# Performance work log

Measured on AMD Instinct MI355X. Metric: run time of the kernel, lower is better.

Reference implementation:

```python
import jax, jax.numpy as jnp
import numpy as np

EMB = 64
HID = 128
N_NODES = 50000
N_EDGES = 800000
N_Q = 64

def setup_inputs() -> dict:
    key = jax.random.key(0)
    ks = jax.random.split(key, 20)
    d = {}
    d['question_emb'] = jax.random.normal(ks[0], (N_Q, EMB), dtype=jnp.float32)
    d['node_embeddings'] = jax.random.normal(ks[1], (N_NODES, EMB), dtype=jnp.float32)
    d['edge_embeddings'] = jax.random.normal(ks[2], (N_EDGES, EMB), dtype=jnp.float32)
    d['edge_index'] = jax.random.randint(ks[3], (2, N_EDGES), 0, N_NODES, dtype=jnp.int32)
    d['node_batch'] = jnp.sort(jax.random.randint(ks[4], (N_NODES,), 0, N_Q, dtype=jnp.int32))
    s = 1.0 / np.sqrt(EMB)
    # projector weights (Linear emb->emb), stored as (in, out)
    d['Wq'] = jax.random.normal(ks[5], (EMB, EMB), dtype=jnp.float32) * s
    d['bq'] = jnp.zeros((EMB,), dtype=jnp.float32)
    d['We'] = jax.random.normal(ks[6], (EMB, EMB), dtype=jnp.float32) * s
    d['be'] = jnp.zeros((EMB,), dtype=jnp.float32)
    d['Wr'] = jax.random.normal(ks[7], (EMB, EMB), dtype=jnp.float32) * s
    d['br'] = jnp.zeros((EMB,), dtype=jnp.float32)
    # DenseFeatureExtractor: concat(4*EMB) -> EMB -> HID, ReLU after each
    d['W1'] = jax.random.normal(ks[8], (4 * EMB, EMB), dtype=jnp.float32) / np.sqrt(4 * EMB)
    d['b1'] = jnp.zeros((EMB,), dtype=jnp.float32)
    d['W2'] = jax.random.normal(ks[9], (EMB, HID), dtype=jnp.float32) * s
    d['b2'] = jnp.zeros((HID,), dtype=jnp.float32)
    # DeterministicHead: HID -> 1
    d['Wh'] = jax.random.normal(ks[10], (HID, 1), dtype=jnp.float32) / np.sqrt(HID)
    d['bh'] = jnp.zeros((1,), dtype=jnp.float32)
    return d


def reference(question_emb, node_embeddings, edge_embeddings, edge_index, node_batch,
              Wq, bq, We, be, Wr, br, W1, b1, W2, b2, Wh, bh):
    head_idx, tail_idx = edge_index[0], edge_index[1]
    query_ids = node_batch[head_idx]                       # [E]
    # projections (applied to the small tables, then gathered per edge)
    q_repr = question_emb @ Wq + bq                        # [Q, D]
    node_repr = node_embeddings @ We + be                  # [N, D]
    rel_repr = edge_embeddings @ Wr + br                   # [E, D]
    semantic = jnp.concatenate([
        q_repr[query_ids], node_repr[head_idx], rel_repr, node_repr[tail_idx]
    ], axis=-1)                                            # [E, 4D]
    h = jax.nn.relu(semantic @ W1 + b1)                    # [E, D]
    h = jax.nn.relu(h @ W2 + b2)                           # [E, H]
    logits = (h @ Wh + bh)[:, 0]                           # [E]
    scores = jax.nn.sigmoid(logits)
    return scores
```

## Files before the change

kernel.cpp:

```cpp
#include <hip/hip_runtime.h>

#define NNODE 50000
#define NEDGE 800000

typedef __attribute__((ext_vector_type(8))) short bf16x8;
typedef __attribute__((ext_vector_type(4))) float f32x4;

#define WB_QCB   0
#define WB_WRTB  8192
#define WB_W2TB  16384
#define WB_WEH   33024
#define WB_WET   49408
#define WB_NHB   65792
#define WB_NTB   6465792

__device__ inline ushort f2b(float x) {
    uint u = __float_as_uint(x);
    return (ushort)((u + 0x7fffu + ((u >> 16) & 1u)) >> 16);
}
__device__ inline float bLo(uint u) { return __uint_as_float(u << 16); }
__device__ inline float bHi(uint u) { return __uint_as_float(u & 0xffff0000u); }

__device__ inline void stage64(float* dst, const float* __restrict__ src, int t) {
    #pragma unroll
    for (int i = 0; i < 4; ++i) {
        int f = t + i * 256;
        *(float4*)&dst[f * 4] = *(const float4*)&src[f * 4];
    }
}

__device__ inline void gemm64(const float* sA, const float* sB, int t, float acc[4][4]) {
    const int r0 = (t >> 4) * 4, c0 = (t & 15) * 4;
    #pragma unroll
    for (int j = 0; j < 4; ++j)
        #pragma unroll
        for (int i = 0; i < 4; ++i) acc[j][i] = 0.f;
    #pragma unroll 4
    for (int k = 0; k < 64; ++k) {
        float4 b = *(const float4*)&sB[k * 64 + c0];
        float bv[4] = {b.x, b.y, b.z, b.w};
        #pragma unroll
        for (int j = 0; j < 4; ++j) {
            float a = sA[(r0 + j) * 64 + k];
            #pragma unroll
            for (int i = 0; i < 4; ++i) acc[j][i] = fmaf(a, bv[i], acc[j][i]);
        }
    }
}

__global__ __launch_bounds__(256)
void prep_small(const float* __restrict__ Q,
                const float* __restrict__ Wq, const float* __restrict__ bq,
                const float* __restrict__ We, const float* __restrict__ be,
                const float* __restrict__ Wr, const float* __restrict__ br,
                const float* __restrict__ W1, const float* __restrict__ b1,
                const float* __restrict__ W2, char* __restrict__ wsb)
{
    __shared__ float sA[4096], sB[4096], sC[4096], sBias[64];
    const int t = threadIdx.x;
    const int bid = blockIdx.x;
    const int r0 = (t >> 4) * 4, c0 = (t & 15) * 4;

    if (bid == 0) {
        stage64(sA, Wq, t); stage64(sB, W1, t);
        __syncthreads();
        float acc[4][4];
        gemm64(sA, sB, t, acc);
        #pragma unroll
        for (int j = 0; j < 4; ++j)
            *(float4*)&sC[(r0 + j) * 64 + c0] = make_float4(acc[j][0], acc[j][1], acc[j][2], acc[j][3]);
        if (t < 64) {
            float s = b1[t];
            for (int k = 0; k < 64; ++k) {
                s = fmaf(bq[k], W1[k * 64 + t], s);
                s = fmaf(be[k], W1[(64 + k) * 64 + t] + W1[(192 + k) * 64 + t], s);
                s = fmaf(br[k], W1[(128 + k) * 64 + t], s);
            }
            sBias[t] = s;
        }
        __syncthreads();
        stage64(sA, Q, t);
        __syncthreads();
        gemm64(sA, sC, t, acc);
        ushort* qcb = (ushort*)(wsb + WB_QCB);
        #pragma unroll
        for (int j = 0; j < 4; ++j) {
            ushort4 p;
            p.x = f2b(acc[j][0] + sBias[c0 + 0]);
            p.y = f2b(acc[j][1] + sBias[c0 + 1]);
            p.z = f2b(acc[j][2] + sBias[c0 + 2]);
            p.w = f2b(acc[j][3] + sBias[c0 + 3]);
            *(ushort4*)&qcb[(r0 + j) * 64 + c0] = p;
        }
    } else if (bid == 1 || bid == 2) {
        const float* w1seg = W1 + (bid == 1 ? 64 * 64 : 192 * 64);
        float* dst = (float*)(wsb + (bid == 1 ? WB_WEH : WB_WET));
        stage64(sA, We, t); stage64(sB, w1seg, t);
        __syncthreads();
        float acc[4][4];
        gemm64(sA, sB, t, acc);
        #pragma unroll
        for (int j = 0; j < 4; ++j)
            *(float4*)&dst[(r0 + j) * 64 + c0] = make_float4(acc[j][0], acc[j][1], acc[j][2], acc[j][3]);
    } else if (bid == 3) {
        stage64(sA, Wr, t); stage64(sB, W1 + 128 * 64, t);
        __syncthreads();
        float acc[4][4];
        gemm64(sA, sB, t, acc);
        ushort* wrtb = (ushort*)(wsb + WB_WRTB);
        #pragma unroll
        for (int j = 0; j < 4; ++j)
            #pragma unroll
            for (int i = 0; i < 4; ++i)
                wrtb[(c0 + i) * 64 + (r0 + j)] = f2b(acc[j][i]);
    } else {
        ushort* w2tb = (ushort*)(wsb + WB_W2TB);
        #pragma unroll
        for (int i = 0; i < 32; ++i) {
            int f = t + i * 256;
            int k = f >> 7, n = f & 127;
            w2tb[n * 64 + k] = f2b(W2[f]);
        }
    }
}

__global__ __launch_bounds__(256)
void prep_nodes(const float* __restrict__ Xn, const char* __restrict__ wsb_c,
                char* __restrict__ wsb)
{
    __shared__ float sXT[64 * 68];
    __shared__ float sWeh[4096], sWet[4096];
    const int t = threadIdx.x;
    const int nbase = blockIdx.x * 64;
    const float* Weh = (const float*)(wsb_c + WB_WEH);
    const float* Wet = (const float*)(wsb_c + WB_WET);
    ushort* nhb = (ushort*)(wsb + WB_NHB);
    ushort* ntb = (ushort*)(wsb + WB_NTB);

    #pragma unroll
    for (int i = 0; i < 4; ++i) {
        int f = t + i * 256;
        int n = f >> 4, s4 = (f & 15) * 4;
        int gn = nbase + n;
        float4 v = make_float4(0.f, 0.f, 0.f, 0.f);
        if (gn < NNODE) v = *(const float4*)&Xn[gn * 64 + s4];
        sXT[(s4 + 0) * 68 + n] = v.x;
        sXT[(s4 + 1) * 68 + n] = v.y;
        sXT[(s4 + 2) * 68 + n] = v.z;
        sXT[(s4 + 3) * 68 + n] = v.w;
    }
    #pragma unroll
    for (int i = 0; i < 4; ++i) {
        int f = t + i * 256;
        *(float4*)&sWeh[f * 4] = *(const float4*)&Weh[f * 4];
        *(float4*)&sWet[f * 4] = *(const float4*)&Wet[f * 4];
    }
    __syncthreads();

    const int er = (t >> 4) * 4, cc = (t & 15) * 4;
    float ah[4][4], at[4][4];
    #pragma unroll
    for (int j = 0; j < 4; ++j)
        #pragma unroll
        for (int i = 0; i < 4; ++i) { ah[j][i] = 0.f; at[j][i] = 0.f; }
    #pragma unroll 4
    for (int k = 0; k < 64; ++k) {
        float4 a  = *(const float4*)&sXT[k * 68 + er];
        float4 bh = *(const float4*)&sWeh[k * 64 + cc];
        float4 bt = *(const float4*)&sWet[k * 64 + cc];
        float av[4] = {a.x, a.y, a.z, a.w};
        #pragma unroll
        for (int j = 0; j < 4; ++j) {
            ah[j][0] = fmaf(av[j], bh.x, ah[j][0]); ah[j][1] = fmaf(av[j], bh.y, ah[j][1]);
            ah[j][2] = fmaf(av[j], bh.z, ah[j][2]); ah[j][3] = fmaf(av[j], bh.w, ah[j][3]);
            at[j][0] = fmaf(av[j], bt.x, at[j][0]); at[j][1] = fmaf(av[j], bt.y, at[j][1]);
            at[j][2] = fmaf(av[j], bt.z, at[j][2]); at[j][3] = fmaf(av[j], bt.w, at[j][3]);
        }
    }
    #pragma unroll
    for (int j = 0; j < 4; ++j) {
        int n = nbase + er + j;
        if (n < NNODE) {
            ushort4 ph, pt;
            ph.x = f2b(ah[j][0]); ph.y = f2b(ah[j][1]); ph.z = f2b(ah[j][2]); ph.w = f2b(ah[j][3]);
            pt.x = f2b(at[j][0]); pt.y = f2b(at[j][1]); pt.z = f2b(at[j][2]); pt.w = f2b(at[j][3]);
            *(ushort4*)&nhb[n * 64 + cc] = ph;
            *(ushort4*)&ntb[n * 64 + cc] = pt;
        }
    }
}

__global__ __launch_bounds__(256, 3)
void edge_kernel(const float* __restrict__ Xe,
                 const int* __restrict__ EI,
                 const int* __restrict__ NB,
                 const float* __restrict__ b2,
                 const float* __restrict__ Wh,
                 const float* __restrict__ bh,
                 const char* __restrict__ wsb,
                 float* __restrict__ out)
{
    __shared__ ushort sX[64 * 72];
    __shared__ ushort sWr[64 * 72];
    __shared__ ushort sW2[128 * 72];
    __shared__ ushort sG[64 * 72];
    __shared__ float  sB2s[128], sWhs[128];

    const int t = threadIdx.x;
    const int ebase = blockIdx.x * 64;
    const ushort* qcb  = (const ushort*)(wsb + WB_QCB);
    const ushort* wrtb = (const ushort*)(wsb + WB_WRTB);
    const ushort* w2tb = (const ushort*)(wsb + WB_W2TB);
    const ushort* nhb  = (const ushort*)(wsb + WB_NHB);
    const ushort* ntb  = (const ushort*)(wsb + WB_NTB);

    const int eg = t >> 2;
    const int c0 = (t & 3) * 16;
    int hd = EI[ebase + eg];
    int tl = EI[NEDGE + ebase + eg];
    int qi = NB[hd];
    uint4 ga0 = *(const uint4*)&qcb[qi * 64 + c0];
    uint4 ga1 = *(const uint4*)&qcb[qi * 64 + c0 + 8];
    uint4 gb0 = *(const uint4*)&nhb[hd * 64 + c0];
    uint4 gb1 = *(const uint4*)&nhb[hd * 64 + c0 + 8];
    uint4 gc0 = *(const uint4*)&ntb[tl * 64 + c0];
    uint4 gc1 = *(const uint4*)&ntb[tl * 64 + c0 + 8];

    float4 xv[4];
    #pragma unroll
    for (int i = 0; i < 4; ++i) {
        int f = t + i * 256;
        xv[i] = *(const float4*)&Xe[(ebase + (f >> 4)) * 64 + (f & 15) * 4];
    }
    uint4 wrl[2], w2l[4];
    #pragma unroll
    for (int i = 0; i < 2; ++i) {
        int f = t + i * 256;
        wrl[i] = *(const uint4*)&wrtb[(f >> 3) * 64 + (f & 7) * 8];
    }
    #pragma unroll
    for (int i = 0; i < 4; ++i) {
        int f = t + i * 256;
        w2l[i] = *(const uint4*)&w2tb[(f >> 3) * 64 + (f & 7) * 8];
    }
    if (t < 128) { sB2s[t] = b2[t]; sWhs[t] = Wh[t]; }
    float bh0 = bh[0];

    {
        uint pk[8];
        const uint* ua = (const uint*)&ga0; const uint* ub = (const uint*)&gb0;
        const uint* uc = (const uint*)&gc0;
        #pragma unroll
        for (int j = 0; j < 4; ++j) {
            float lo = bLo(ua[j]) + bLo(ub[j]) + bLo(uc[j]);
            float hi = bHi(ua[j]) + bHi(ub[j]) + bHi(uc[j]);
            pk[j] = (uint)f2b(lo) | ((uint)f2b(hi) << 16);
        }
        ua = (const uint*)&ga1; ub = (const uint*)&gb1; uc = (const uint*)&gc1;
        #pragma unroll
        for (int j = 0; j < 4; ++j) {
            float lo = bLo(ua[j]) + bLo(ub[j]) + bLo(uc[j]);
            float hi = bHi(ua[j]) + bHi(ub[j]) + bHi(uc[j]);
            pk[4 + j] = (uint)f2b(lo) | ((uint)f2b(hi) << 16);
        }
        *(uint4*)&sG[eg * 72 + c0]     = make_uint4(pk[0], pk[1], pk[2], pk[3]);
        *(uint4*)&sG[eg * 72 + c0 + 8] = make_uint4(pk[4], pk[5], pk[6], pk[7]);
    }
    #pragma unroll
    for (int i = 0; i < 4; ++i) {
        int f = t + i * 256;
        int e = f >> 4, s4 = (f & 15) * 4;
        uint lo = (uint)f2b(xv[i].x) | ((uint)f2b(xv[i].y) << 16);
        uint hi = (uint)f2b(xv[i].z) | ((uint)f2b(xv[i].w) << 16);
        *(uint2*)&sX[e * 72 + s4] = make_uint2(lo, hi);
    }
    #pragma unroll
    for (int i = 0; i < 2; ++i) {
        int f = t + i * 256;
        *(uint4*)&sWr[(f >> 3) * 72 + (f & 7) * 8] = wrl[i];
    }
    #pragma unroll
    for (int i = 0; i < 4; ++i) {
        int f = t + i * 256;
        *(uint4*)&sW2[(f >> 3) * 72 + (f & 7) * 8] = w2l[i];
    }
    __syncthreads();

    const int lane = t & 63;
    const int w = t >> 6;
    const int m = lane & 15;
    const int qq = lane >> 4;
    const int q8 = qq * 8;

    bf16x8 a0 = *(const bf16x8*)&sX[(w * 16 + m) * 72 + q8];
    bf16x8 a1 = *(const bf16x8*)&sX[(w * 16 + m) * 72 + 32 + q8];
    f32x4 acc1[4];
    #pragma unroll
    for (int nt = 0; nt < 4; ++nt) {
        bf16x8 b0 = *(const bf16x8*)&sWr[(nt * 16 + m) * 72 + q8];
        bf16x8 b1v = *(const bf16x8*)&sWr[(nt * 16 + m) * 72 + 32 + q8];
        f32x4 c = {0.f, 0.f, 0.f, 0.f};
        c = __builtin_amdgcn_mfma_f32_16x16x32_bf16(a0, b0, c, 0, 0, 0);
        c = __builtin_amdgcn_mfma_f32_16x16x32_bf16(a1, b1v, c, 0, 0, 0);
        acc1[nt] = c;
    }
    ushort h1s[4][4];
    #pragma unroll
    for (int nt = 0; nt < 4; ++nt) {
        int c = nt * 16 + m;
        #pragma unroll
        for (int r = 0; r < 4; ++r) {
            int e = w * 16 + qq * 4 + r;
            float gv = __uint_as_float(((uint)sG[e * 72 + c]) << 16);
            h1s[nt][r] = f2b(fmaxf(acc1[nt][r] + gv, 0.f));
        }
    }
    __syncthreads();
    #pragma unroll
    for (int nt = 0; nt < 4; ++nt) {
        int c = nt * 16 + m;
        #pragma unroll
        for (int r = 0; r < 4; ++r) {
            int e = w * 16 + qq * 4 + r;
            sX[e * 72 + c] = h1s[nt][r];
        }
    }
    __syncthreads();

    bf16x8 A0 = *(const bf16x8*)&sX[(w * 16 + m) * 72 + q8];
    bf16x8 A1 = *(const bf16x8*)&sX[(w * 16 + m) * 72 + 32 + q8];
    float part[4] = {0.f, 0.f, 0.f, 0.f};
    #pragma unroll
    for (int nt = 0; nt < 8; ++nt) {
        bf16x8 B0 = *(const bf16x8*)&sW2[(nt * 16 + m) * 72 + q8];
        bf16x8 B1 = *(const bf16x8*)&sW2[(nt * 16 + m) * 72 + 32 + q8];
        f32x4 c = {0.f, 0.f, 0.f, 0.f};
        c = __builtin_amdgcn_mfma_f32_16x16x32_bf16(A0, B0, c, 0, 0, 0);
        c = __builtin_amdgcn_mfma_f32_16x16x32_bf16(A1, B1, c, 0, 0, 0);
        int col = nt * 16 + m;
        float b2v = sB2s[col], whv = sWhs[col];
        #pragma unroll
        for (int r = 0; r < 4; ++r)
            part[r] = fmaf(fmaxf(c[r] + b2v, 0.f), whv, part[r]);
    }
    #pragma unroll
    for (int md = 1; md < 16; md <<= 1) {
        part[0] += __shfl_xor(part[0], md, 64);
        part[1] += __shfl_xor(part[1], md, 64);
        part[2] += __shfl_xor(part[2], md, 64);
        part[3] += __shfl_xor(part[3], md, 64);
    }
    if (m == 0) {
        float4 o;
        o.x = 1.f / (1.f + __expf(-(part[0] + bh0)));
        o.y = 1.f / (1.f + __expf(-(part[1] + bh0)));
        o.z = 1.f / (1.f + __expf(-(part[2] + bh0)));
        o.w = 1.f / (1.f + __expf(-(part[3] + bh0)));
        *(float4*)&out[ebase + w * 16 + qq * 4] = o;
    }
}

extern "C" void kernel_launch(void* const* d_in, const int* in_sizes, int n_in,
                              void* d_out, int out_size, void* d_ws, size_t ws_size,
                              hipStream_t stream)
{
    const float* Q   = (const float*)d_in[0];
    const float* Xn  = (const float*)d_in[1];
    const float* Xe  = (const float*)d_in[2];
    const int*   EI  = (const int*)d_in[3];
    const int*   NB  = (const int*)d_in[4];
    const float* Wq  = (const float*)d_in[5];
    const float* bq  = (const float*)d_in[6];
    const float* We  = (const float*)d_in[7];
    const float* be  = (const float*)d_in[8];
    const float* Wr  = (const float*)d_in[9];
    const float* br  = (const float*)d_in[10];
    const float* W1  = (const float*)d_in[11];
    const float* b1  = (const float*)d_in[12];
    const float* W2  = (const float*)d_in[13];
    const float* b2  = (const float*)d_in[14];
    const float* Wh  = (const float*)d_in[15];
    const float* bh  = (const float*)d_in[16];
    float* out = (float*)d_out;
    char*  wsb = (char*)d_ws;

    prep_small<<<5, 256, 0, stream>>>(Q, Wq, bq, We, be, Wr, br, W1, b1, W2, wsb);
    prep_nodes<<<(NNODE + 63) / 64, 256, 0, stream>>>(Xn, wsb, wsb);
    edge_kernel<<<NEDGE / 64, 256, 0, stream>>>(Xe, EI, NB, b2, Wh, bh, wsb, out);
}
```

Before: 375.1 us.

## Load MFMA operands directly into registers and permute hidden layout to cut LDS syncs

The edge kernel now loads the edge-embedding A fragments and Wr B fragments straight from global memory into registers in MFMA layout, so the sX and sWr shared buffers are gone. The gathered sum is stored in a permuted column order, and W2 rows are permuted to match. This lets each wave write its first-layer output to a wave-private sH region with packed stores and read it back with no extra block barriers. Less LDS is used, so occupancy is raised to 4 blocks per SIMD, at the cost of uncoalesced per-lane global loads and more register pressure.

```diff
diff --git a/kernel.cpp b/kernel.cpp
--- a/kernel.cpp
+++ b/kernel.cpp
@@ -18,8 +18,13 @@
     uint u = __float_as_uint(x);
     return (ushort)((u + 0x7fffu + ((u >> 16) & 1u)) >> 16);
 }
+__device__ inline uint pack2(float lo, float hi) {
+    return (uint)f2b(lo) | ((uint)f2b(hi) << 16);
+}
 __device__ inline float bLo(uint u) { return __uint_as_float(u << 16); }
 __device__ inline float bHi(uint u) { return __uint_as_float(u & 0xffff0000u); }
+
+union B8U { uint4 u; bf16x8 b; };
 
 __device__ inline void stage64(float* dst, const float* __restrict__ src, int t) {
     #pragma unroll
@@ -119,7 +124,7 @@
         for (int i = 0; i < 32; ++i) {
             int f = t + i * 256;
             int k = f >> 7, n = f & 127;
-            w2tb[n * 64 + k] = f2b(W2[f]);
+            w2tb[n * 64 + ((k & 15) * 4 + (k >> 4))] = f2b(W2[f]);
         }
     }
 }
@@ -190,7 +195,7 @@
     }
 }
 
-__global__ __launch_bounds__(256, 3)
+__global__ __launch_bounds__(256, 4)
 void edge_kernel(const float* __restrict__ Xe,
                  const int* __restrict__ EI,
                  const int* __restrict__ NB,
@@ -200,135 +205,100 @@
                  const char* __restrict__ wsb,
                  float* __restrict__ out)
 {
-    __shared__ ushort sX[64 * 72];
-    __shared__ ushort sWr[64 * 72];
+    __shared__ ushort sG[64 * 72];
+    __shared__ ushort sH[64 * 72];
     __shared__ ushort sW2[128 * 72];
-    __shared__ ushort sG[64 * 72];
     __shared__ float  sB2s[128], sWhs[128];
 
     const int t = threadIdx.x;
     const int ebase = blockIdx.x * 64;
+    const int l = t & 63, w = t >> 6;
+    const int m = l & 15, qq = l >> 4, q8 = qq * 8;
+
     const ushort* qcb  = (const ushort*)(wsb + WB_QCB);
     const ushort* wrtb = (const ushort*)(wsb + WB_WRTB);
     const ushort* w2tb = (const ushort*)(wsb + WB_W2TB);
     const ushort* nhb  = (const ushort*)(wsb + WB_NHB);
     const ushort* ntb  = (const ushort*)(wsb + WB_NTB);
 
-    const int eg = t >> 2;
-    const int c0 = (t & 3) * 16;
+    const int eg = w * 16 + (l >> 2);
+    const int qg = l & 3;
     int hd = EI[ebase + eg];
     int tl = EI[NEDGE + ebase + eg];
     int qi = NB[hd];
-    uint4 ga0 = *(const uint4*)&qcb[qi * 64 + c0];
-    uint4 ga1 = *(const uint4*)&qcb[qi * 64 + c0 + 8];
-    uint4 gb0 = *(const uint4*)&nhb[hd * 64 + c0];
-    uint4 gb1 = *(const uint4*)&nhb[hd * 64 + c0 + 8];
-    uint4 gc0 = *(const uint4*)&ntb[tl * 64 + c0];
-    uint4 gc1 = *(const uint4*)&ntb[tl * 64 + c0 + 8];
-
-    float4 xv[4];
+
+    const float* xrow = &Xe[(size_t)(ebase + w * 16 + m) * 64];
+    float4 x0 = *(const float4*)&xrow[q8];
+    float4 x1 = *(const float4*)&xrow[q8 + 4];
+    float4 x2 = *(const float4*)&xrow[32 + q8];
+    float4 x3 = *(const float4*)&xrow[32 + q8 + 4];
+
+    B8U wrB[4][2];
+    #pragma unroll
+    for (int nt = 0; nt < 4; ++nt) {
+        const ushort* row = &wrtb[(nt * 16 + m) * 64];
+        wrB[nt][0].u = *(const uint4*)&row[q8];
+        wrB[nt][1].u = *(const uint4*)&row[32 + q8];
+    }
+
     #pragma unroll
     for (int i = 0; i < 4; ++i) {
         int f = t + i * 256;
-        xv[i] = *(const float4*)&Xe[(ebase + (f >> 4)) * 64 + (f & 15) * 4];
-    }
-    uint4 wrl[2], w2l[4];
-    #pragma unroll
-    for (int i = 0; i < 2; ++i) {
-        int f = t + i * 256;
-        wrl[i] = *(const uint4*)&wrtb[(f >> 3) * 64 + (f & 7) * 8];
-    }
-    #pragma unroll
-    for (int i = 0; i < 4; ++i) {
-        int f = t + i * 256;
-        w2l[i] = *(const uint4*)&w2tb[(f >> 3) * 64 + (f & 7) * 8];
+        *(uint4*)&sW2[(f >> 3) * 72 + (f & 7) * 8] = *(const uint4*)&w2tb[f * 8];
     }
     if (t < 128) { sB2s[t] = b2[t]; sWhs[t] = Wh[t]; }
     float bh0 = bh[0];
 
     {
+        float s[16];
+        #pragma unroll
+        for (int a = 0; a < 4; ++a) {
+            int coff = a * 16 + qg * 4;
+            uint2 gq = *(const uint2*)&qcb[qi * 64 + coff];
+            uint2 gh = *(const uint2*)&nhb[(size_t)hd * 64 + coff];
+            uint2 gt = *(const uint2*)&ntb[(size_t)tl * 64 + coff];
+            s[a]      = bLo(gq.x) + bLo(gh.x) + bLo(gt.x);
+            s[4 + a]  = bHi(gq.x) + bHi(gh.x) + bHi(gt.x);
+            s[8 + a]  = bLo(gq.y) + bLo(gh.y) + bLo(gt.y);
+            s[12 + a] = bHi(gq.y) + bHi(gh.y) + bHi(gt.y);
+        }
         uint pk[8];
-        const uint* ua = (const uint*)&ga0; const uint* ub = (const uint*)&gb0;
-        const uint* uc = (const uint*)&gc0;
-        #pragma unroll
-        for (int j = 0; j < 4; ++j) {
-            float lo = bLo(ua[j]) + bLo(ub[j]) + bLo(uc[j]);
-            float hi = bHi(ua[j]) + bHi(ub[j]) + bHi(uc[j]);
-            pk[j] = (uint)f2b(lo) | ((uint)f2b(hi) << 16);
-        }
-        ua = (const uint*)&ga1; ub = (const uint*)&gb1; uc = (const uint*)&gc1;
-        #pragma unroll
-        for (int j = 0; j < 4; ++j) {
-            float lo = bLo(ua[j]) + bLo(ub[j]) + bLo(uc[j]);
-            float hi = bHi(ua[j]) + bHi(ub[j]) + bHi(uc[j]);
-            pk[4 + j] = (uint)f2b(lo) | ((uint)f2b(hi) << 16);
-        }
-        *(uint4*)&sG[eg * 72 + c0]     = make_uint4(pk[0], pk[1], pk[2], pk[3]);
-        *(uint4*)&sG[eg * 72 + c0 + 8] = make_uint4(pk[4], pk[5], pk[6], pk[7]);
-    }
-    #pragma unroll
-    for (int i = 0; i < 4; ++i) {
-        int f = t + i * 256;
-        int e = f >> 4, s4 = (f & 15) * 4;
-        uint lo = (uint)f2b(xv[i].x) | ((uint)f2b(xv[i].y) << 16);
-        uint hi = (uint)f2b(xv[i].z) | ((uint)f2b(xv[i].w) << 16);
-        *(uint2*)&sX[e * 72 + s4] = make_uint2(lo, hi);
-    }
-    #pragma unroll
-    for (int i = 0; i < 2; ++i) {
-        int f = t + i * 256;
-        *(uint4*)&sWr[(f >> 3) * 72 + (f & 7) * 8] = wrl[i];
-    }
-    #pragma unroll
-    for (int i = 0; i < 4; ++i) {
-        int f = t + i * 256;
-        *(uint4*)&sW2[(f >> 3) * 72 + (f & 7) * 8] = w2l[i];
-    }
+        #pragma unroll
+        for (int wd = 0; wd < 8; ++wd) pk[wd] = pack2(s[2 * wd], s[2 * wd + 1]);
+        *(uint4*)&sG[eg * 72 + qg * 16]     = make_uint4(pk[0], pk[1], pk[2], pk[3]);
+        *(uint4*)&sG[eg * 72 + qg * 16 + 8] = make_uint4(pk[4], pk[5], pk[6], pk[7]);
+    }
+
+    B8U a0, a1;
+    a0.u = make_uint4(pack2(x0.x, x0.y), pack2(x0.z, x0.w),
+                      pack2(x1.x, x1.y), pack2(x1.z, x1.w));
+    a1.u = make_uint4(pack2(x2.x, x2.y), pack2(x2.z, x2.w),
+                      pack2(x3.x, x3.y), pack2(x3.z, x3.w));
+
     __syncthreads();
 
-    const int lane = t & 63;
-    const int w = t >> 6;
-    const int m = lane & 15;
-    const int qq = lane >> 4;
-    const int q8 = qq * 8;
-
-    bf16x8 a0 = *(const bf16x8*)&sX[(w * 16 + m) * 72 + q8];
-    bf16x8 a1 = *(const bf16x8*)&sX[(w * 16 + m) * 72 + 32 + q8];
     f32x4 acc1[4];
     #pragma unroll
     for (int nt = 0; nt < 4; ++nt) {
-        bf16x8 b0 = *(const bf16x8*)&sWr[(nt * 16 + m) * 72 + q8];
-        bf16x8 b1v = *(const bf16x8*)&sWr[(nt * 16 + m) * 72 + 32 + q8];
         f32x4 c = {0.f, 0.f, 0.f, 0.f};
-        c = __builtin_amdgcn_mfma_f32_16x16x32_bf16(a0, b0, c, 0, 0, 0);
-        c = __builtin_amdgcn_mfma_f32_16x16x32_bf16(a1, b1v, c, 0, 0, 0);
+        c = __builtin_amdgcn_mfma_f32_16x16x32_bf16(a0.b, wrB[nt][0].b, c, 0, 0, 0);
+        c = __builtin_amdgcn_mfma_f32_16x16x32_bf16(a1.b, wrB[nt][1].b, c, 0, 0, 0);
         acc1[nt] = c;
     }
-    ushort h1s[4][4];
-    #pragma unroll
-    for (int nt = 0; nt < 4; ++nt) {
-        int c = nt * 16 + m;
-        #pragma unroll
-        for (int r = 0; r < 4; ++r) {
-            int e = w * 16 + qq * 4 + r;
-            float gv = __uint_as_float(((uint)sG[e * 72 + c]) << 16);
-            h1s[nt][r] = f2b(fmaxf(acc1[nt][r] + gv, 0.f));
-        }
-    }
-    __syncthreads();
-    #pragma unroll
-    for (int nt = 0; nt < 4; ++nt) {
-        int c = nt * 16 + m;
-        #pragma unroll
-        for (int r = 0; r < 4; ++r) {
-            int e = w * 16 + qq * 4 + r;
-            sX[e * 72 + c] = h1s[nt][r];
-        }
-    }
-    __syncthreads();
-
-    bf16x8 A0 = *(const bf16x8*)&sX[(w * 16 + m) * 72 + q8];
-    bf16x8 A1 = *(const bf16x8*)&sX[(w * 16 + m) * 72 + 32 + q8];
+
+    #pragma unroll
+    for (int r = 0; r < 4; ++r) {
+        int e = w * 16 + qq * 4 + r;
+        uint2 gg = *(const uint2*)&sG[e * 72 + m * 4];
+        uint lo = pack2(fmaxf(acc1[0][r] + bLo(gg.x), 0.f),
+                        fmaxf(acc1[1][r] + bHi(gg.x), 0.f));
+        uint hi = pack2(fmaxf(acc1[2][r] + bLo(gg.y), 0.f),
+                        fmaxf(acc1[3][r] + bHi(gg.y), 0.f));
+        *(uint2*)&sH[e * 72 + m * 4] = make_uint2(lo, hi);
+    }
+
+    bf16x8 A0 = *(const bf16x8*)&sH[(w * 16 + m) * 72 + q8];
+    bf16x8 A1 = *(const bf16x8*)&sH[(w * 16 + m) * 72 + 32 + q8];
     float part[4] = {0.f, 0.f, 0.f, 0.f};
     #pragma unroll
     for (int nt = 0; nt < 8; ++nt) {
```

Result: slower. 388.2 us (+3.5%).
